# Kernel tuning notes

Measured on AMD Instinct MI355X. Metric: run time of the kernel, lower is better.

## Reference

```python
import jax, jax.numpy as jnp
import numpy as np

EMBED_DIM = 1024
NUM_HEADS = 16
HEAD_DIM = EMBED_DIM // NUM_HEADS


def setup_inputs() -> dict:
    key = jax.random.key(0)
    kx, kw1, kb1, kw2, kb2 = jax.random.split(key, 5)
    D = EMBED_DIM
    # torch nn.Linear default init: U(-1/sqrt(in), 1/sqrt(in)); use scaled uniform
    lim = 1.0 / np.sqrt(D)
    return {
        "x": jax.random.normal(kx, (2, 2048, D), dtype=jnp.float32),
        "w_qkv": jax.random.uniform(kw1, (D, 3 * D), jnp.float32, -lim, lim),
        "b_qkv": jax.random.uniform(kb1, (3 * D,), jnp.float32, -lim, lim),
        "w_o": jax.random.uniform(kw2, (D, D), jnp.float32, -lim, lim),
        "b_o": jax.random.uniform(kb2, (D,), jnp.float32, -lim, lim),
    }


def reference(x, w_qkv, b_qkv, w_o, b_o):
    B, S, D = x.shape
    H, hd = NUM_HEADS, HEAD_DIM
    qkv = x @ w_qkv + b_qkv                       # [B,S,3D]
    qkv = qkv.reshape(B, S, H, 3, hd)             # per-head [q|k|v] blocks of size hd
    q = qkv[:, :, :, 0].transpose(0, 2, 1, 3)     # [B,H,S,hd]
    k = qkv[:, :, :, 1].transpose(0, 2, 1, 3)
    v = qkv[:, :, :, 2].transpose(0, 2, 1, 3)
    scale = hd ** -0.5
    scores = jnp.einsum('bhqd,bhkd->bhqk', q, k) * scale
    attn = jax.nn.softmax(scores, axis=-1)
    out = jnp.einsum('bhqk,bhkd->bhqd', attn, v)  # [B,H,S,hd]
    out = out.transpose(0, 2, 1, 3).reshape(B, S, D)
    return out @ w_o + b_o
```

## Files before the change

kernel.cpp:

```cpp
#include <hip/hip_runtime.h>

typedef __attribute__((ext_vector_type(8))) _Float16 half8;
typedef __attribute__((ext_vector_type(4))) _Float16 half4;
typedef __attribute__((ext_vector_type(4))) float f32x4;
typedef __attribute__((ext_vector_type(16))) float f32x16;
typedef __attribute__((ext_vector_type(4))) int i32x4;

typedef __attribute__((address_space(1))) void* gptr_t;
typedef __attribute__((address_space(3))) void* lptr_t;
#define GLL16(g, l) __builtin_amdgcn_global_load_lds((gptr_t)(g), (lptr_t)(l), 16, 0, 0)

__device__ __forceinline__ float fast_exp2(float x) {
  float r;
  asm volatile("v_exp_f32 %0, %1" : "=v"(r) : "v"(x));
  return r;
}


__global__ void cvt_x_kernel(const float* __restrict__ x, _Float16* __restrict__ xh) {
  size_t i = (size_t)blockIdx.x * blockDim.x + threadIdx.x;
  float4 v = *reinterpret_cast<const float4*>(x + i * 4);
  half4 o = { (_Float16)v.x, (_Float16)v.y, (_Float16)v.z, (_Float16)v.w };
  *reinterpret_cast<half4*>(xh + i * 4) = o;
}

__global__ void transpose_cvt_kernel(const float* __restrict__ w, _Float16* __restrict__ wt, int N) {
  int tid = blockIdx.x * blockDim.x + threadIdx.x;
  int n = tid % N, kc = tid / N;
  half8 o;
#pragma unroll
  for (int i = 0; i < 8; ++i) o[i] = (_Float16)w[(size_t)(kc * 8 + i) * N + n];
  *reinterpret_cast<half8*>(wt + (size_t)n * 1024 + kc * 8) = o;
}


template<int EPI>
__global__ __launch_bounds__(256, 2)
void gemm16(const _Float16* __restrict__ A, const _Float16* __restrict__ Bt,
            const float* __restrict__ bias,
            _Float16* __restrict__ qh, _Float16* __restrict__ kh,
            _Float16* __restrict__ vT, float* __restrict__ outf) {
  __shared__ __align__(16) _Float16 Ah[128 * 64];
  __shared__ __align__(16) _Float16 Bh[128 * 64];
  const int t = threadIdx.x;
  const int w = t >> 6, ln = t & 63, G = ln >> 4, c = ln & 15;
  const int m0 = blockIdx.y * 128, n0 = blockIdx.x * 128;
  const int wr = w >> 1, wc = w & 1;
  f32x4 acc[4][4] = {};
  for (int kt = 0; kt < 1024; kt += 64) {
#pragma unroll
    for (int i = 0; i < 4; ++i) {
      int ch = i * 256 + t;
      int row = ch >> 3, kc = ch & 7;
      int kk = kt + ((kc ^ (row & 7)) << 3);
      int ldsbase = (i * 256 + w * 64) * 8;
      GLL16(A + (size_t)(m0 + row) * 1024 + kk, Ah + ldsbase);
      GLL16(Bt + (size_t)(n0 + row) * 1024 + kk, Bh + ldsbase);
    }
    __syncthreads();
    half8 aF[2][4], bF[2][4];
#pragma unroll
    for (int ks = 0; ks < 2; ++ks)
#pragma unroll
      for (int i = 0; i < 4; ++i) {
        int ra = wr * 64 + i * 16 + c;
        aF[ks][i] = *reinterpret_cast<const half8*>(&Ah[ra * 64 + (((ks * 4 + G) ^ (ra & 7)) << 3)]);
        int rb = wc * 64 + i * 16 + c;
        bF[ks][i] = *reinterpret_cast<const half8*>(&Bh[rb * 64 + (((ks * 4 + G) ^ (rb & 7)) << 3)]);
      }
#pragma unroll
    for (int ks = 0; ks < 2; ++ks)
#pragma unroll
      for (int mi = 0; mi < 4; ++mi)
#pragma unroll
        for (int ni = 0; ni < 4; ++ni)
          acc[mi][ni] = __builtin_amdgcn_mfma_f32_16x16x32_f16(aF[ks][mi], bF[ks][ni], acc[mi][ni], 0, 0, 0);
    __syncthreads();
  }
  const int mbase = m0 + wr * 64, nbase = n0 + wc * 64;
  const int Gp = ((G & 1) << 1) | (G >> 1);
#pragma unroll
  for (int ni = 0; ni < 4; ++ni) {
    int n = nbase + ni * 16 + c;
    float bv = bias[n];
    if (EPI == 0) {
      int h = n / 192;
      int rem = n - h * 192;
      int tt = rem >> 6, d = rem & 63;
#pragma unroll
      for (int mi = 0; mi < 4; ++mi) {
        if (tt == 2) {
          int mb = mbase + mi * 16;
          int bb = mb >> 11, s0 = mb & 2047;
          size_t bh = (size_t)(bb * 16 + h);
          half4 o = { (_Float16)(acc[mi][ni][0] + bv), (_Float16)(acc[mi][ni][1] + bv),
                      (_Float16)(acc[mi][ni][2] + bv), (_Float16)(acc[mi][ni][3] + bv) };
          *reinterpret_cast<half4*>(&vT[(bh * 64 + d) * 2048 + s0 + 4 * Gp]) = o;
        } else {
#pragma unroll
          for (int r = 0; r < 4; ++r) {
            int m = mbase + mi * 16 + 4 * G + r;
            int bb = m >> 11, s = m & 2047;
            float val = acc[mi][ni][r] + bv;
            size_t bh = (size_t)(bb * 16 + h);
            if (tt == 0) qh[(bh * 2048 + s) * 64 + d] = (_Float16)(val * (0.125f * 1.44269504089f));
            else         kh[(bh * 2048 + s) * 64 + d] = (_Float16)val;
          }
        }
      }
    } else {
#pragma unroll
      for (int mi = 0; mi < 4; ++mi)
#pragma unroll
        for (int r = 0; r < 4; ++r) {
          int m = mbase + mi * 16 + 4 * G + r;
          outf[(size_t)m * 1024 + n] = acc[mi][ni][r] + bv;
        }
    }
  }
}


__global__ __launch_bounds__(256, 2)
void attn_kernel(const _Float16* __restrict__ qh, const _Float16* __restrict__ kh,
                 const _Float16* __restrict__ vT, _Float16* __restrict__ ao) {
  __shared__ __align__(16) _Float16 Kt[2][64 * 64];
  __shared__ __align__(16) _Float16 Vt[3][64 * 64];
  const int t = threadIdx.x;
  const int w = t >> 6, ln = t & 63, lo = ln & 31, hi = ln >> 5;
  const int bid = blockIdx.x;
  const int xcd = bid & 7, tt = bid >> 3;
  const int bh = xcd * 4 + (tt >> 4);
  const int qb = tt & 15;
  const int q0 = qb * 128 + w * 32;
  const _Float16* qp = qh + (size_t)bh * 2048 * 64;
  const _Float16* kp = kh + (size_t)bh * 2048 * 64;
  const _Float16* vp = vT + (size_t)bh * 64 * 2048;

  half8 qf[4];
#pragma unroll
  for (int sl = 0; sl < 4; ++sl)
    qf[sl] = *reinterpret_cast<const half8*>(qp + (size_t)(q0 + lo) * 64 + sl * 16 + hi * 8);

  f32x16 O0 = {}, O1 = {};
  float plsum = 0.f;
  unsigned pk[4][4];

  auto stage = [&](int kb, int vb3, int jt) {
#pragma unroll
    for (int i = 0; i < 2; ++i) {
      int ch = i * 256 + t;
      int row = ch >> 3, cc = ch & 7;
      int sw = ((cc ^ (row & 7)) << 3);
      int ldsbase = (i * 256 + w * 64) * 8;
      GLL16(kp + (size_t)(jt + row) * 64 + sw, &Kt[kb][ldsbase]);
      GLL16(vp + (size_t)row * 2048 + jt + sw, &Vt[vb3][ldsbase]);
    }
  };

  auto qkt = [&](int kb, f32x16& s0, f32x16& s1) {
#pragma unroll
    for (int sl = 0; sl < 4; ++sl) {
      const int ch = sl * 2 + hi;
      const int sw = (ch ^ (lo & 7)) << 3;
      half8 k0 = *reinterpret_cast<const half8*>(&Kt[kb][lo * 64 + sw]);
      s0 = __builtin_amdgcn_mfma_f32_32x32x16_f16(k0, qf[sl], s0, 0, 0, 0);
      half8 k1 = *reinterpret_cast<const half8*>(&Kt[kb][(32 + lo) * 64 + sw]);
      s1 = __builtin_amdgcn_mfma_f32_32x32x16_f16(k1, qf[sl], s1, 0, 0, 0);
    }
  };

  auto pv = [&](int vb3) {
#pragma unroll
    for (int kb2 = 0; kb2 < 4; ++kb2) {
      i32x4 pi = { (int)pk[kb2][0], (int)pk[kb2][1], (int)pk[kb2][2], (int)pk[kb2][3] };
      half8 pf = __builtin_bit_cast(half8, pi);
      const int ch = kb2 * 2 + hi;
      const int sw = (ch ^ (lo & 7)) << 3;
      half8 v0 = *reinterpret_cast<const half8*>(&Vt[vb3][lo * 64 + sw]);
      O0 = __builtin_amdgcn_mfma_f32_32x32x16_f16(v0, pf, O0, 0, 0, 0);
      half8 v1 = *reinterpret_cast<const half8*>(&Vt[vb3][(32 + lo) * 64 + sw]);
      O1 = __builtin_amdgcn_mfma_f32_32x32x16_f16(v1, pf, O1, 0, 0, 0);
    }
  };

  auto smpack = [&](f32x16& s0, f32x16& s1) {
#pragma unroll
    for (int i = 0; i < 16; ++i) s0[i] = fast_exp2(s0[i]);
#pragma unroll
    for (int i = 0; i < 16; ++i) s1[i] = fast_exp2(s1[i]);
    float sm[8];
#pragma unroll
    for (int i = 0; i < 8; ++i) sm[i] = (s0[i] + s0[i + 8]) + (s1[i] + s1[i + 8]);
#pragma unroll
    for (int i = 0; i < 4; ++i) sm[i] += sm[i + 4];
    plsum += (sm[0] + sm[1]) + (sm[2] + sm[3]);
#pragma unroll
    for (int kh2 = 0; kh2 < 2; ++kh2)
#pragma unroll
      for (int j = 0; j < 4; ++j) {
        pk[kh2][j]     = __builtin_bit_cast(unsigned, __builtin_amdgcn_cvt_pkrtz(s0[kh2 * 8 + 2 * j], s0[kh2 * 8 + 2 * j + 1]));
        pk[2 + kh2][j] = __builtin_bit_cast(unsigned, __builtin_amdgcn_cvt_pkrtz(s1[kh2 * 8 + 2 * j], s1[kh2 * 8 + 2 * j + 1]));
      }
  };

  stage(0, 0, 0);
  stage(1, 1, 64);
  __syncthreads();
  {
    f32x16 s0 = {}, s1 = {};
    qkt(0, s0, s1);
    smpack(s0, s1);
  }
  __syncthreads();

  for (int it = 0; it < 31; ++it) {
    if (it < 30) {
      int vb2 = it + 2; vb2 -= (vb2 >= 3 ? 3 : 0); vb2 -= (vb2 >= 3 ? 3 : 0);
      stage(it & 1, (it + 2) % 3, (it + 2) * 64);
    }
    f32x16 s0 = {}, s1 = {};
    __builtin_amdgcn_s_setprio(1);
    qkt((it + 1) & 1, s0, s1);
    pv(it % 3);
    __builtin_amdgcn_s_setprio(0);
    smpack(s0, s1);
    __syncthreads();
  }
  pv(31 % 3);

  float lsum = plsum + __shfl_xor(plsum, 32);
  float inv = 1.f / lsum;
  const int bb = bh >> 4, hd_i = bh & 15;
  const size_t srow = (size_t)bb * 2048 + q0 + lo;
  _Float16* aob = ao + srow * 1024 + hd_i * 64 + hi * 4;
#pragma unroll
  for (int rq = 0; rq < 4; ++rq) {
    half4 o0 = { (_Float16)(O0[4 * rq] * inv), (_Float16)(O0[4 * rq + 1] * inv),
                 (_Float16)(O0[4 * rq + 2] * inv), (_Float16)(O0[4 * rq + 3] * inv) };
    *reinterpret_cast<half4*>(aob + rq * 8) = o0;
    half4 o1 = { (_Float16)(O1[4 * rq] * inv), (_Float16)(O1[4 * rq + 1] * inv),
                 (_Float16)(O1[4 * rq + 2] * inv), (_Float16)(O1[4 * rq + 3] * inv) };
    *reinterpret_cast<half4*>(aob + 32 + rq * 8) = o1;
  }
}


extern "C" void kernel_launch(void* const* d_in, const int* in_sizes, int n_in,
                              void* d_out, int out_size, void* d_ws, size_t ws_size,
                              hipStream_t stream) {
  const float* x     = (const float*)d_in[0];
  const float* w_qkv = (const float*)d_in[1];
  const float* b_qkv = (const float*)d_in[2];
  const float* w_o   = (const float*)d_in[3];
  const float* b_o   = (const float*)d_in[4];
  float* out = (float*)d_out;
  char* ws = (char*)d_ws;
  _Float16* xh    = (_Float16*)(ws);
  _Float16* wqkvT = (_Float16*)(ws + ((size_t)8  << 20));
  _Float16* woT   = (_Float16*)(ws + ((size_t)14 << 20));
  _Float16* qh    = (_Float16*)(ws + ((size_t)16 << 20));
  _Float16* kh    = (_Float16*)(ws + ((size_t)24 << 20));
  _Float16* vT    = (_Float16*)(ws + ((size_t)32 << 20));
  _Float16* ao    = (_Float16*)(ws + ((size_t)40 << 20));

  cvt_x_kernel<<<4096, 256, 0, stream>>>(x, xh);
  transpose_cvt_kernel<<<1536, 256, 0, stream>>>(w_qkv, wqkvT, 3072);
  transpose_cvt_kernel<<<512, 256, 0, stream>>>(w_o, woT, 1024);
  gemm16<0><<<dim3(24, 32), 256, 0, stream>>>(xh, wqkvT, b_qkv, qh, kh, vT, nullptr);
  attn_kernel<<<512, 256, 0, stream>>>(qh, kh, vT, ao);
  gemm16<1><<<dim3(8, 32), 256, 0, stream>>>(ao, woT, b_o, nullptr, nullptr, nullptr, out);
}
```

Baseline: 128.3 us.

## Load attention K/V directly to registers, tile weight transpose via LDS, shrink out-proj tiles

The attention kernel drops its LDS staging and barriers, loading K and V fragments straight from global memory into registers with a double-buffered K prefetch. The weight transpose-convert kernel now goes through an LDS tile so both global reads and writes are coalesced. The output projection gets its own GEMM with 128x64 tiles, doubling the block count to 512 for better CU fill. The risks are more global load traffic and higher load latency in attention without LDS reuse across waves, plus extra register pressure.

```diff
diff --git a/kernel.cpp b/kernel.cpp
--- a/kernel.cpp
+++ b/kernel.cpp
@@ -25,21 +25,35 @@
 }
 
 __global__ void transpose_cvt_kernel(const float* __restrict__ w, _Float16* __restrict__ wt, int N) {
-  int tid = blockIdx.x * blockDim.x + threadIdx.x;
-  int n = tid % N, kc = tid / N;
-  half8 o;
-#pragma unroll
-  for (int i = 0; i < 8; ++i) o[i] = (_Float16)w[(size_t)(kc * 8 + i) * N + n];
-  *reinterpret_cast<half8*>(wt + (size_t)n * 1024 + kc * 8) = o;
-}
-
-
-template<int EPI>
+  __shared__ _Float16 lds[64][72];
+  const int t = threadIdx.x;
+  const int n0 = blockIdx.x * 64, k0 = blockIdx.y * 64;
+#pragma unroll
+  for (int rep = 0; rep < 4; ++rep) {
+    int k = rep * 16 + (t >> 4);
+    int nc = (t & 15) * 4;
+    float4 v = *reinterpret_cast<const float4*>(&w[(size_t)(k0 + k) * N + n0 + nc]);
+    lds[nc + 0][k] = (_Float16)v.x;
+    lds[nc + 1][k] = (_Float16)v.y;
+    lds[nc + 2][k] = (_Float16)v.z;
+    lds[nc + 3][k] = (_Float16)v.w;
+  }
+  __syncthreads();
+#pragma unroll
+  for (int rep = 0; rep < 2; ++rep) {
+    int ch = rep * 256 + t;
+    int n = ch >> 3, kc = ch & 7;
+    half8 o = *reinterpret_cast<const half8*>(&lds[n][kc * 8]);
+    *reinterpret_cast<half8*>(&wt[(size_t)(n0 + n) * 1024 + k0 + kc * 8]) = o;
+  }
+}
+
+
 __global__ __launch_bounds__(256, 2)
-void gemm16(const _Float16* __restrict__ A, const _Float16* __restrict__ Bt,
-            const float* __restrict__ bias,
-            _Float16* __restrict__ qh, _Float16* __restrict__ kh,
-            _Float16* __restrict__ vT, float* __restrict__ outf) {
+void gemm_qkv(const _Float16* __restrict__ A, const _Float16* __restrict__ Bt,
+              const float* __restrict__ bias,
+              _Float16* __restrict__ qh, _Float16* __restrict__ kh,
+              _Float16* __restrict__ vT) {
   __shared__ __align__(16) _Float16 Ah[128 * 64];
   __shared__ __align__(16) _Float16 Bh[128 * 64];
   const int t = threadIdx.x;
@@ -83,40 +97,95 @@
   for (int ni = 0; ni < 4; ++ni) {
     int n = nbase + ni * 16 + c;
     float bv = bias[n];
-    if (EPI == 0) {
-      int h = n / 192;
-      int rem = n - h * 192;
-      int tt = rem >> 6, d = rem & 63;
-#pragma unroll
-      for (int mi = 0; mi < 4; ++mi) {
-        if (tt == 2) {
-          int mb = mbase + mi * 16;
-          int bb = mb >> 11, s0 = mb & 2047;
-          size_t bh = (size_t)(bb * 16 + h);
-          half4 o = { (_Float16)(acc[mi][ni][0] + bv), (_Float16)(acc[mi][ni][1] + bv),
-                      (_Float16)(acc[mi][ni][2] + bv), (_Float16)(acc[mi][ni][3] + bv) };
-          *reinterpret_cast<half4*>(&vT[(bh * 64 + d) * 2048 + s0 + 4 * Gp]) = o;
-        } else {
-#pragma unroll
-          for (int r = 0; r < 4; ++r) {
-            int m = mbase + mi * 16 + 4 * G + r;
-            int bb = m >> 11, s = m & 2047;
-            float val = acc[mi][ni][r] + bv;
-            size_t bh = (size_t)(bb * 16 + h);
-            if (tt == 0) qh[(bh * 2048 + s) * 64 + d] = (_Float16)(val * (0.125f * 1.44269504089f));
-            else         kh[(bh * 2048 + s) * 64 + d] = (_Float16)val;
-          }
-        }
-      }
-    } else {
-#pragma unroll
-      for (int mi = 0; mi < 4; ++mi)
+    int h = n / 192;
+    int rem = n - h * 192;
+    int tt = rem >> 6, d = rem & 63;
+#pragma unroll
+    for (int mi = 0; mi < 4; ++mi) {
+      if (tt == 2) {
+        int mb = mbase + mi * 16;
+        int bb = mb >> 11, s0 = mb & 2047;
+        size_t bh = (size_t)(bb * 16 + h);
+        half4 o = { (_Float16)(acc[mi][ni][0] + bv), (_Float16)(acc[mi][ni][1] + bv),
+                    (_Float16)(acc[mi][ni][2] + bv), (_Float16)(acc[mi][ni][3] + bv) };
+        *reinterpret_cast<half4*>(&vT[(bh * 64 + d) * 2048 + s0 + 4 * Gp]) = o;
+      } else {
 #pragma unroll
         for (int r = 0; r < 4; ++r) {
           int m = mbase + mi * 16 + 4 * G + r;
-          outf[(size_t)m * 1024 + n] = acc[mi][ni][r] + bv;
+          int bb = m >> 11, s = m & 2047;
+          float val = acc[mi][ni][r] + bv;
+          size_t bh = (size_t)(bb * 16 + h);
+          if (tt == 0) qh[(bh * 2048 + s) * 64 + d] = (_Float16)(val * (0.125f * 1.44269504089f));
+          else         kh[(bh * 2048 + s) * 64 + d] = (_Float16)val;
         }
-    }
+      }
+    }
+  }
+}
+
+
+__global__ __launch_bounds__(256, 2)
+void gemm_o(const _Float16* __restrict__ A, const _Float16* __restrict__ Bt,
+            const float* __restrict__ bias, float* __restrict__ outf) {
+  __shared__ __align__(16) _Float16 Ah[128 * 64];
+  __shared__ __align__(16) _Float16 Bh[64 * 64];
+  const int t = threadIdx.x;
+  const int w = t >> 6, ln = t & 63, G = ln >> 4, c = ln & 15;
+  const int m0 = blockIdx.y * 128, n0 = blockIdx.x * 64;
+  const int wr = w >> 1, wc = w & 1;
+  f32x4 acc[4][2] = {};
+  for (int kt = 0; kt < 1024; kt += 64) {
+#pragma unroll
+    for (int i = 0; i < 4; ++i) {
+      int ch = i * 256 + t;
+      int row = ch >> 3, kc = ch & 7;
+      int kk = kt + ((kc ^ (row & 7)) << 3);
+      GLL16(A + (size_t)(m0 + row) * 1024 + kk, Ah + (i * 256 + w * 64) * 8);
+    }
+#pragma unroll
+    for (int i = 0; i < 2; ++i) {
+      int ch = i * 256 + t;
+      int row = ch >> 3, kc = ch & 7;
+      int kk = kt + ((kc ^ (row & 7)) << 3);
+      GLL16(Bt + (size_t)(n0 + row) * 1024 + kk, Bh + (i * 256 + w * 64) * 8);
+    }
+    __syncthreads();
+    half8 aF[2][4], bF[2][2];
+#pragma unroll
+    for (int ks = 0; ks < 2; ++ks) {
+#pragma unroll
+      for (int i = 0; i < 4; ++i) {
+        int ra = wr * 64 + i * 16 + c;
+        aF[ks][i] = *reinterpret_cast<const half8*>(&Ah[ra * 64 + (((ks * 4 + G) ^ (ra & 7)) << 3)]);
+      }
+#pragma unroll
+      for (int i = 0; i < 2; ++i) {
+        int rb = wc * 32 + i * 16 + c;
+        bF[ks][i] = *reinterpret_cast<const half8*>(&Bh[rb * 64 + (((ks * 4 + G) ^ (rb & 7)) << 3)]);
+      }
+    }
+#pragma unroll
+    for (int ks = 0; ks < 2; ++ks)
+#pragma unroll
+      for (int mi = 0; mi < 4; ++mi)
+#pragma unroll
+        for (int ni = 0; ni < 2; ++ni)
+          acc[mi][ni] = __builtin_amdgcn_mfma_f32_16x16x32_f16(aF[ks][mi], bF[ks][ni], acc[mi][ni], 0, 0, 0);
+    __syncthreads();
+  }
+  const int mbase = m0 + wr * 64, nbase = n0 + wc * 32;
+#pragma unroll
+  for (int ni = 0; ni < 2; ++ni) {
+    int n = nbase + ni * 16 + c;
+    float bv = bias[n];
+#pragma unroll
+    for (int mi = 0; mi < 4; ++mi)
+#pragma unroll
+      for (int r = 0; r < 4; ++r) {
+        int m = mbase + mi * 16 + 4 * G + r;
+        outf[(size_t)m * 1024 + n] = acc[mi][ni][r] + bv;
+      }
   }
 }
 
@@ -124,8 +193,6 @@
 __global__ __launch_bounds__(256, 2)
 void attn_kernel(const _Float16* __restrict__ qh, const _Float16* __restrict__ kh,
                  const _Float16* __restrict__ vT, _Float16* __restrict__ ao) {
-  __shared__ __align__(16) _Float16 Kt[2][64 * 64];
-  __shared__ __align__(16) _Float16 Vt[3][64 * 64];
   const int t = threadIdx.x;
   const int w = t >> 6, ln = t & 63, lo = ln & 31, hi = ln >> 5;
   const int bid = blockIdx.x;
@@ -134,8 +201,8 @@
   const int qb = tt & 15;
   const int q0 = qb * 128 + w * 32;
   const _Float16* qp = qh + (size_t)bh * 2048 * 64;
-  const _Float16* kp = kh + (size_t)bh * 2048 * 64;
-  const _Float16* vp = vT + (size_t)bh * 64 * 2048;
+  const _Float16* kbase = kh + (size_t)bh * 2048 * 64 + (size_t)lo * 64 + hi * 8;
+  const _Float16* vbase = vT + (size_t)bh * 64 * 2048 + (size_t)lo * 2048 + hi * 8;
 
   half8 qf[4];
 #pragma unroll
@@ -146,42 +213,43 @@
   float plsum = 0.f;
   unsigned pk[4][4];
 
-  auto stage = [&](int kb, int vb3, int jt) {
-#pragma unroll
-    for (int i = 0; i < 2; ++i) {
-      int ch = i * 256 + t;
-      int row = ch >> 3, cc = ch & 7;
-      int sw = ((cc ^ (row & 7)) << 3);
-      int ldsbase = (i * 256 + w * 64) * 8;
-      GLL16(kp + (size_t)(jt + row) * 64 + sw, &Kt[kb][ldsbase]);
-      GLL16(vp + (size_t)row * 2048 + jt + sw, &Vt[vb3][ldsbase]);
-    }
-  };
-
-  auto qkt = [&](int kb, f32x16& s0, f32x16& s1) {
+  auto loadK = [&](int tile, half8 kf[2][4]) {
+    const _Float16* p = kbase + (size_t)tile * 4096;
+#pragma unroll
+    for (int h2 = 0; h2 < 2; ++h2)
+#pragma unroll
+      for (int sl = 0; sl < 4; ++sl)
+        kf[h2][sl] = *reinterpret_cast<const half8*>(p + h2 * 2048 + sl * 16);
+  };
+  auto loadV = [&](int tile, half8 vf[2][4]) {
+    const _Float16* p = vbase + tile * 64;
+#pragma unroll
+    for (int dh = 0; dh < 2; ++dh)
+#pragma unroll
+      for (int kb2 = 0; kb2 < 4; ++kb2)
+        vf[dh][kb2] = *reinterpret_cast<const half8*>(p + dh * 65536 + kb2 * 16);
+  };
+
+  auto qkt = [&](const half8 kf[2][4], f32x16& s0, f32x16& s1) {
+    __builtin_amdgcn_s_setprio(1);
 #pragma unroll
     for (int sl = 0; sl < 4; ++sl) {
-      const int ch = sl * 2 + hi;
-      const int sw = (ch ^ (lo & 7)) << 3;
-      half8 k0 = *reinterpret_cast<const half8*>(&Kt[kb][lo * 64 + sw]);
-      s0 = __builtin_amdgcn_mfma_f32_32x32x16_f16(k0, qf[sl], s0, 0, 0, 0);
-      half8 k1 = *reinterpret_cast<const half8*>(&Kt[kb][(32 + lo) * 64 + sw]);
-      s1 = __builtin_amdgcn_mfma_f32_32x32x16_f16(k1, qf[sl], s1, 0, 0, 0);
-    }
-  };
-
-  auto pv = [&](int vb3) {
+      s0 = __builtin_amdgcn_mfma_f32_32x32x16_f16(kf[0][sl], qf[sl], s0, 0, 0, 0);
+      s1 = __builtin_amdgcn_mfma_f32_32x32x16_f16(kf[1][sl], qf[sl], s1, 0, 0, 0);
+    }
+    __builtin_amdgcn_s_setprio(0);
+  };
+
+  auto pv = [&](const half8 vf[2][4]) {
+    __builtin_amdgcn_s_setprio(1);
 #pragma unroll
     for (int kb2 = 0; kb2 < 4; ++kb2) {
       i32x4 pi = { (int)pk[kb2][0], (int)pk[kb2][1], (int)pk[kb2][2], (int)pk[kb2][3] };
       half8 pf = __builtin_bit_cast(half8, pi);
-      const int ch = kb2 * 2 + hi;
-      const int sw = (ch ^ (lo & 7)) << 3;
-      half8 v0 = *reinterpret_cast<const half8*>(&Vt[vb3][lo * 64 + sw]);
-      O0 = __builtin_amdgcn_mfma_f32_32x32x16_f16(v0, pf, O0, 0, 0, 0);
-      half8 v1 = *reinterpret_cast<const half8*>(&Vt[vb3][(32 + lo) * 64 + sw]);
-      O1 = __builtin_amdgcn_mfma_f32_32x32x16_f16(v1, pf, O1, 0, 0, 0);
-    }
+      O0 = __builtin_amdgcn_mfma_f32_32x32x16_f16(vf[0][kb2], pf, O0, 0, 0, 0);
+      O1 = __builtin_amdgcn_mfma_f32_32x32x16_f16(vf[1][kb2], pf, O1, 0, 0, 0);
+    }
+    __builtin_amdgcn_s_setprio(0);
   };
 
   auto smpack = [&](f32x16& s0, f32x16& s1) {
@@ -204,30 +272,26 @@
       }
   };
 
-  stage(0, 0, 0);
-  stage(1, 1, 64);
-  __syncthreads();
-  {
-    f32x16 s0 = {}, s1 = {};
-    qkt(0, s0, s1);
-    smpack(s0, s1);
-  }
-  __syncthreads();
-
-  for (int it = 0; it < 31; ++it) {
-    if (it < 30) {
-      int vb2 = it + 2; vb2 -= (vb2 >= 3 ? 3 : 0); vb2 -= (vb2 >= 3 ? 3 : 0);
-      stage(it & 1, (it + 2) % 3, (it + 2) * 64);
-    }
-    f32x16 s0 = {}, s1 = {};
-    __builtin_amdgcn_s_setprio(1);
-    qkt((it + 1) & 1, s0, s1);
-    pv(it % 3);
-    __builtin_amdgcn_s_setprio(0);
-    smpack(s0, s1);
-    __syncthreads();
-  }
-  pv(31 % 3);
+  half8 kfA[2][4], kfB[2][4], vf[2][4];
+  loadK(0, kfA);
+  for (int it = 0; it < 32; it += 2) {
+    loadK(it + 1, kfB);
+    loadV(it, vf);
+    {
+      f32x16 s0 = {}, s1 = {};
+      qkt(kfA, s0, s1);
+      smpack(s0, s1);
+      pv(vf);
+    }
+    loadK(it + 2, kfA);
+    loadV(it + 1, vf);
+    {
+      f32x16 s0 = {}, s1 = {};
+      qkt(kfB, s0, s1);
+      smpack(s0, s1);
+      pv(vf);
+    }
+  }
 
   float lsum = plsum + __shfl_xor(plsum, 32);
   float inv = 1.f / lsum;
@@ -265,9 +329,9 @@
   _Float16* ao    = (_Float16*)(ws + ((size_t)40 << 20));
 
   cvt_x_kernel<<<4096, 256, 0, stream>>>(x, xh);
-  transpose_cvt_kernel<<<1536, 256, 0, stream>>>(w_qkv, wqkvT, 3072);
-  transpose_cvt_kernel<<<512, 256, 0, stream>>>(w_o, woT, 1024);
-  gemm16<0><<<dim3(24, 32), 256, 0, stream>>>(xh, wqkvT, b_qkv, qh, kh, vT, nullptr);
+  transpose_cvt_kernel<<<dim3(48, 16), 256, 0, stream>>>(w_qkv, wqkvT, 3072);
+  transpose_cvt_kernel<<<dim3(16, 16), 256, 0, stream>>>(w_o, woT, 1024);
+  gemm_qkv<<<dim3(24, 32), 256, 0, stream>>>(xh, wqkvT, b_qkv, qh, kh, vT);
   attn_kernel<<<512, 256, 0, stream>>>(qh, kh, vT, ao);
-  gemm16<1><<<dim3(8, 32), 256, 0, stream>>>(ao, woT, b_o, nullptr, nullptr, nullptr, out);
-}
+  gemm_o<<<dim3(16, 32), 256, 0, stream>>>(ao, woT, b_o, out);
+}
```

Measured after the change: 194.1 us. 1.51x slower.
